# Optimization experiments

Hardware: AMD Instinct MI355X
Metric: run time of the kernel (lower is better)

The kernel has to match this reference:

```python
import jax, jax.numpy as jnp
import numpy as np

H = 256          # hidden_dim
I = 128          # input_dim
R = 32           # mod_rank
B = 16           # batch
T = 48           # timesteps
CLIP_VAL = 1.0
LN_EPS = 1e-5


def _ln(y, g, b):
    mu = jnp.mean(y, axis=-1, keepdims=True)
    var = jnp.mean((y - mu) ** 2, axis=-1, keepdims=True)
    return (y - mu) * jax.lax.rsqrt(var + LN_EPS) * g + b


def setup_inputs() -> dict:
    key = jax.random.key(0)
    ks = jax.random.split(key, 8)
    inp = {
        "x": jax.random.normal(ks[0], (T, B, I), jnp.float32),
        "h": jnp.zeros((B, H), jnp.float32),
        "v": jnp.zeros((B, H), jnp.float32),
        "dU": jnp.zeros((B, H, H), jnp.float32),
        "trace_e": jnp.zeros((B, H), jnp.float32),
        "trace_E": jnp.zeros((B, H, H), jnp.float32),
        # parameters (kaiming-ish scales; biases per reset_parameter)
        "W_x2h": jax.random.normal(ks[1], (3 * H, I), jnp.float32) * np.sqrt(2.0 / I),
        "b_x2h": jnp.zeros((3 * H,), jnp.float32),
        "W_h2h": jax.random.normal(ks[2], (3 * H, H), jnp.float32) * np.sqrt(2.0 / H),
        "b_h2h": jnp.concatenate([-jnp.ones((2 * H,)), jnp.zeros((H,))]).astype(jnp.float32),
        "ln_x_g": jnp.ones((3 * H,), jnp.float32),
        "ln_x_b": jnp.zeros((3 * H,), jnp.float32),
        "ln_h_g": jnp.ones((3 * H,), jnp.float32),
        "ln_h_b": jnp.zeros((3 * H,), jnp.float32),
        "W_h2mod": jax.random.normal(ks[3], (R, H), jnp.float32) * np.sqrt(2.0 / H),
        "b_h2mod": jnp.zeros((R,), jnp.float32),
        "W_mod2h": jax.random.normal(ks[4], (2, R), jnp.float32) * np.sqrt(2.0 / R),
        "b_mod2h": jnp.zeros((2,), jnp.float32),
        "alpha": jnp.full((1,), -4.5, jnp.float32),
        "tau_U": jnp.full((1,), -3.0, jnp.float32),
    }
    return inp


def reference(x, h, v, dU, trace_e, trace_E, W_x2h, b_x2h, W_h2h, b_h2h,
              ln_x_g, ln_x_b, ln_h_g, ln_h_b, W_h2mod, b_h2mod,
              W_mod2h, b_mod2h, alpha, tau_U):
    sp_a = jax.nn.softplus(alpha)                    # [1]
    tau = jax.nn.sigmoid(tau_U)                      # [1]
    Wv_slice = W_h2h[2 * H:3 * H, :]                 # [H,H]
    upper = jax.nn.relu(CLIP_VAL - Wv_slice) / sp_a  # [H,H], >= 0
    lower = -jax.nn.relu(CLIP_VAL + Wv_slice) / sp_a # [H,H], <= 0

    def step(carry, x_t):
        h, v, dU, te, tE = carry
        Wx = _ln(x_t @ W_x2h.T + b_x2h, ln_x_g, ln_x_b)          # [B,3H]
        Wh = h @ W_h2h.T + b_h2h                                  # [B,3H]
        plastic = sp_a * jnp.einsum('bij,bj->bi', dU, h)          # [B,H]
        Wh = Wh.at[:, 2 * H:].add(plastic)
        Wh = _ln(Wh, ln_h_g, ln_h_b)
        pre = Wx + Wh
        z = jax.nn.sigmoid(pre[:, :H])
        r = jax.nn.sigmoid(pre[:, H:2 * H])
        dv = pre[:, 2 * H:]
        v_new = (1.0 - z) * v + z * dv
        h_new = jax.nn.relu(v_new)                                # activation='relu'
        mod = jax.nn.relu(h_new @ W_h2mod.T + b_h2mod)            # [B,R]
        sm = mod @ W_mod2h.T + b_mod2h                            # [B,2]
        s = jax.nn.sigmoid(sm[:, 0:1])[:, :, None]                # [B,1,1]
        m = sm[:, 1:2][:, :, None]                                # [B,1,1]
        te_new = (1.0 - r) * te + r * h
        outer = (h_new[:, :, None] * te_new[:, None, :]
                 - te_new[:, :, None] * h_new[:, None, :])        # [B,H,H] antisym
        tE_new = (1.0 - s) * tE + s * outer
        dU_new = (1.0 - tau) * dU + tau * m * tE_new
        dU_new = jnp.minimum(dU_new, upper[None])
        dU_new = jnp.maximum(dU_new, lower[None])
        return (h_new, v_new, dU_new, te_new, tE_new), (h_new, mod)

    (h, v, dU, trace_e, trace_E), (outs, mods) = jax.lax.scan(
        step, (h, v, dU, trace_e, trace_E), x)
    return v, h, dU, trace_e, trace_E, outs, mods
```

## Files before the change

### kernel.cpp

```cpp
#include <hip/hip_runtime.h>

#define H_  256
#define I_  128
#define R_  32
#define B_  16
#define T_  48
#define H3_ 768

#define OFF_V    0
#define OFF_H    4096
#define OFF_DU   8192
#define OFF_TE   1056768
#define OFF_TT   1060864
#define OFF_OUTS 2109440
#define OFF_MODS 2306048

#define BAR_STRIDE 32

typedef unsigned long long u64;

__device__ __align__(16) float g_wx[T_*B_*H3_];
__device__ __align__(16) u64 g_whp[2*B_*H3_];
__device__ __align__(16) u64 g_plp[2*B_*H_];
__device__ int g_bar[B_*BAR_STRIDE];
__device__ int g_done[B_*BAR_STRIDE];

__device__ __forceinline__ float sigmf(float v){ return 1.0f/(1.0f+__expf(-v)); }

__device__ __forceinline__ void pstore(u64* p, int tag, float v){
  u64 u = ((u64)(unsigned)tag << 32) | (u64)__float_as_uint(v);
  __hip_atomic_store(p, u, __ATOMIC_RELAXED, __HIP_MEMORY_SCOPE_AGENT);
}
__device__ __forceinline__ u64 pload(const u64* p){
  return __hip_atomic_load((u64*)p, __ATOMIC_RELAXED, __HIP_MEMORY_SCOPE_AGENT);
}
__device__ __forceinline__ void pload4_l2(const u64* p0, const u64* p1,
                                          const u64* p2, const u64* p3,
                                          u64& u0, u64& u1, u64& u2, u64& u3){
  asm volatile(
    "global_load_dwordx2 %0, %4, off sc0\n\t"
    "global_load_dwordx2 %1, %5, off sc0\n\t"
    "global_load_dwordx2 %2, %6, off sc0\n\t"
    "global_load_dwordx2 %3, %7, off sc0\n\t"
    "s_waitcnt vmcnt(0)"
    : "=&v"(u0), "=&v"(u1), "=&v"(u2), "=&v"(u3)
    : "v"(p0), "v"(p1), "v"(p2), "v"(p3)
    : "memory");
}

__device__ __forceinline__ void groupbar_full(int* ctr, int target){
  __syncthreads();
  if (threadIdx.x == 0){
    __threadfence();
    __hip_atomic_fetch_add(ctr, 1, __ATOMIC_RELAXED, __HIP_MEMORY_SCOPE_AGENT);
    while (__hip_atomic_load(ctr, __ATOMIC_RELAXED, __HIP_MEMORY_SCOPE_AGENT) < target)
      __builtin_amdgcn_s_sleep(1);
    __threadfence();
  }
  __syncthreads();
}

__global__ __launch_bounds__(256, 1) void sgru_kernel(
    const float* __restrict__ x,     const float* __restrict__ h0,
    const float* __restrict__ v0,    const float* __restrict__ dU0,
    const float* __restrict__ te0,   const float* __restrict__ tE0,
    const float* __restrict__ Wx2h,  const float* __restrict__ bx2h,
    const float* __restrict__ Wh2h,  const float* __restrict__ bh2h,
    const float* __restrict__ lnxg,  const float* __restrict__ lnxb,
    const float* __restrict__ lnhg,  const float* __restrict__ lnhb,
    const float* __restrict__ Wh2mod,const float* __restrict__ bh2mod,
    const float* __restrict__ Wmod2h,const float* __restrict__ bmod2h,
    const float* __restrict__ alpha, const float* __restrict__ tauU,
    float* __restrict__ out)
{
  const int tid  = threadIdx.x;
  const int g    = blockIdx.x;
  const int b    = (g & 7) + 8*(g >> 7);
  const int c    = (g >> 3) & 15;
  const int lane = tid & 63;
  const int wv   = tid >> 6;

  __shared__ __align__(16) float hn_s[H_], ten_s[H_];
  __shared__ __align__(16) float xst_s[3*I_];
  __shared__ __align__(16) float lnhg_s[H3_], lnhb_s[H3_];
  __shared__ __align__(16) float wrow_s[48*256];
  __shared__ float mod_s[R_];
  __shared__ float red_s[8];

  float* ws_wx = g_wx;
  int*   ctr   = g_bar  + b*BAR_STRIDE;
  int*   dctr  = g_done + b*BAR_STRIDE;

  const float sp_a    = log1pf(__expf(alpha[0]));
  const float inv_spa = 1.0f / sp_a;
  const float tau     = sigmf(tauU[0]);

  float h_r  = h0[b*H_+tid];
  float v_r  = v0[b*H_+tid];
  float te_r = te0[b*H_+tid];
  hn_s[tid] = h_r;
  for (int idx = tid; idx < 48*64; idx += 256){
    int d = idx >> 6, j = idx & 63;
    float4 w4 = ((const float4*)(Wh2h + ((size_t)(c*48 + d))*H_))[j];
    ((float4*)wrow_s)[(d>>4)*1024 + (j>>2)*64 + (d&15)*4 + (j&3)] = w4;
  }
  for (int idx = tid; idx < H3_; idx += 256){
    lnhg_s[idx] = lnhg[idx];
    lnhb_s[idx] = lnhb[idx];
  }
  float4 upR[4], loR[4];
  float4 duR[4], tER[4];
  #pragma unroll
  for (int rr = 0; rr < 4; rr++){
    int i = c*16 + rr*4 + wv;
    float4 w = ((const float4*)(Wh2h + ((size_t)(2*H_ + i))*H_))[lane];
    upR[rr].x =  fmaxf(1.0f - w.x, 0.0f)*inv_spa;
    upR[rr].y =  fmaxf(1.0f - w.y, 0.0f)*inv_spa;
    upR[rr].z =  fmaxf(1.0f - w.z, 0.0f)*inv_spa;
    upR[rr].w =  fmaxf(1.0f - w.w, 0.0f)*inv_spa;
    loR[rr].x = -fmaxf(1.0f + w.x, 0.0f)*inv_spa;
    loR[rr].y = -fmaxf(1.0f + w.y, 0.0f)*inv_spa;
    loR[rr].z = -fmaxf(1.0f + w.z, 0.0f)*inv_spa;
    loR[rr].w = -fmaxf(1.0f + w.w, 0.0f)*inv_spa;
    size_t rowo = ((size_t)(b*H_ + i))*H_;
    duR[rr] = ((const float4*)(dU0 + rowo))[lane];
    tER[rr] = ((const float4*)(tE0 + rowo))[lane];
  }
  const int mk = tid >> 3;
  const int l8 = tid & 7;
  float4 wm[8];
  #pragma unroll
  for (int j = 0; j < 8; j++)
    wm[j] = ((const float4*)(Wh2mod + (size_t)mk*H_))[j*8 + l8];
  const float bh2m = bh2mod[mk];
  const float wmA = Wmod2h[lane & 31];
  const float wmB = Wmod2h[R_ + (lane & 31)];
  const float bm0 = bmod2h[0], bm1 = bmod2h[1];
  float bh2h_reg = 0.f;
  if (tid < 192) bh2h_reg = bh2h[c*48 + (tid>>2)];
  __syncthreads();

  {
    float* xr = xst_s;
    for (int idx = tid; idx < 3*I_; idx += 256){
      int q = idx >> 7, e = idx & 127;
      xr[q*I_ + e] = x[((size_t)((c*3+q)*B_ + b))*I_ + e];
    }
    __syncthreads();
    float acc[3][3];
    #pragma unroll
    for (int k = 0; k < 3; k++){
      acc[k][0]=0.f; acc[k][1]=0.f; acc[k][2]=0.f;
      int f = tid + 256*k;
      const float4* wr = (const float4*)(Wx2h + (size_t)f*I_);
      for (int e4 = 0; e4 < I_/4; e4++){
        float4 w4 = wr[e4];
        int e = e4*4;
        #pragma unroll
        for (int q = 0; q < 3; q++){
          float t0 = fmaf(w4.x, xr[q*I_+e],   acc[k][q]);
          t0       = fmaf(w4.y, xr[q*I_+e+1], t0);
          t0       = fmaf(w4.z, xr[q*I_+e+2], t0);
          acc[k][q]= fmaf(w4.w, xr[q*I_+e+3], t0);
        }
      }
      float bf = bx2h[f];
      acc[k][0]+=bf; acc[k][1]+=bf; acc[k][2]+=bf;
    }
    __syncthreads();
    for (int q = 0; q < 3; q++){
      float s1 = acc[0][q]+acc[1][q]+acc[2][q];
      float s2 = acc[0][q]*acc[0][q]+acc[1][q]*acc[1][q]+acc[2][q]*acc[2][q];
      #pragma unroll
      for (int off=32; off>0; off>>=1){ s1 += __shfl_xor(s1,off); s2 += __shfl_xor(s2,off); }
      if (lane==0){ red_s[wv]=s1; red_s[4+wv]=s2; }
      __syncthreads();
      s1 = red_s[0]+red_s[1]+red_s[2]+red_s[3];
      s2 = red_s[4]+red_s[5]+red_s[6]+red_s[7];
      __syncthreads();
      float mu  = s1*(1.0f/768.0f);
      float var = s2*(1.0f/768.0f) - mu*mu;
      float rs  = rsqrtf(var + 1e-5f);
      float* dst = ws_wx + ((size_t)((c*3+q)*B_ + b))*H3_;
      #pragma unroll
      for (int k = 0; k < 3; k++){
        int f = tid + 256*k;
        dst[f] = (acc[k][q]-mu)*rs*lnxg[f] + lnxb[f];
      }
    }
  }

  {
    const float4* h4 = (const float4*)hn_s;
    float4 hj = h4[lane];
    float a[4];
    #pragma unroll
    for (int rr = 0; rr < 4; rr++){
      float4 du = duR[rr];
      a[rr] = du.x*hj.x + du.y*hj.y + du.z*hj.z + du.w*hj.w;
    }
    #pragma unroll
    for (int off=32; off>0; off>>=1){
      a[0] += __shfl_xor(a[0],off); a[1] += __shfl_xor(a[1],off);
      a[2] += __shfl_xor(a[2],off); a[3] += __shfl_xor(a[3],off);
    }
    if (lane==0){
      #pragma unroll
      for (int rr = 0; rr < 4; rr++)
        pstore(&g_plp[b*H_ + c*16 + rr*4 + wv], 0, sp_a*a[rr]);
    }
    if (tid < 192){
      const int w  = tid >> 6;
      const int l4 = lane & 3;
      const float4* wb  = ((const float4*)wrow_s) + w*1024;
      const float4* hh4 = (const float4*)hn_s;
      float acc = 0.f;
      #pragma unroll
      for (int u = 0; u < 16; u++){
        float4 w4 = wb[u*64 + lane];
        float4 hv = hh4[u*4 + l4];
        acc = fmaf(w4.x,hv.x, fmaf(w4.y,hv.y, fmaf(w4.z,hv.z, fmaf(w4.w,hv.w, acc))));
      }
      acc += __shfl_xor(acc,1);
      acc += __shfl_xor(acc,2);
      if (l4==0) pstore(&g_whp[b*H3_ + c*48 + w*16 + (lane>>2)], 0, acc + bh2h_reg);
    }
  }
  groupbar_full(ctr, 16);

  for (int t = 0; t < T_; t++){
    const int p  = t & 1;
    const int pn = p ^ 1;

    const float* wxr = ws_wx + ((size_t)(t*B_ + b))*H3_;
    float wx0 = wxr[tid], wx1 = wxr[tid+256], wx2 = wxr[tid+512];

    const u64* whp = g_whp + p*(B_*H3_) + b*H3_;
    const u64* plp = g_plp + p*(B_*H_)  + b*H_;
    u64 u0, u1, u2, u3;
    int round = 0;
    for(;;){
      if ((round & 1) == 0){
        pload4_l2(whp+tid, whp+tid+256, whp+tid+512, plp+tid, u0, u1, u2, u3);
      } else {
        u0 = pload(whp + tid);
        u1 = pload(whp + tid + 256);
        u2 = pload(whp + tid + 512);
        u3 = pload(plp + tid);
      }
      bool ok = ((int)(u0>>32)==t) && ((int)(u1>>32)==t) &&
                ((int)(u2>>32)==t) && ((int)(u3>>32)==t);
      if (__all(ok)) break;
      round++;
    }
    float wh0 = __uint_as_float((unsigned)u0);
    float wh1 = __uint_as_float((unsigned)u1);
    float wh2 = __uint_as_float((unsigned)u2) + __uint_as_float((unsigned)u3);

    float hn, ten;
    {
      float s1 = wh0+wh1+wh2;
      float s2 = wh0*wh0+wh1*wh1+wh2*wh2;
      #pragma unroll
      for (int off=32; off>0; off>>=1){ s1 += __shfl_xor(s1,off); s2 += __shfl_xor(s2,off); }
      if (lane==0){ red_s[wv]=s1; red_s[4+wv]=s2; }
      __syncthreads();
      s1 = red_s[0]+red_s[1]+red_s[2]+red_s[3];
      s2 = red_s[4]+red_s[5]+red_s[6]+red_s[7];
      float mu  = s1*(1.0f/768.0f);
      float var = s2*(1.0f/768.0f) - mu*mu;
      float rs  = rsqrtf(var + 1e-5f);
      float pre0 = wx0 + (wh0-mu)*rs*lnhg_s[tid]     + lnhb_s[tid];
      float pre1 = wx1 + (wh1-mu)*rs*lnhg_s[tid+256] + lnhb_s[tid+256];
      float pre2 = wx2 + (wh2-mu)*rs*lnhg_s[tid+512] + lnhb_s[tid+512];
      float z   = sigmf(pre0);
      float r   = sigmf(pre1);
      float vn  = fmaf(z, pre2 - v_r, v_r);
      hn  = fmaxf(vn, 0.0f);
      ten = fmaf(r, h_r - te_r, te_r);
      v_r = vn; h_r = hn; te_r = ten;
      hn_s[tid] = hn; ten_s[tid] = ten;
    }
    __syncthreads();

    const float4* hn4 = (const float4*)hn_s;
    const float4* te4 = (const float4*)ten_s;
    float4 hj = hn4[lane];
    float4 tj = te4[lane];
    float hni[4], teni[4];
    #pragma unroll
    for (int rr = 0; rr < 4; rr++){
      int i = c*16 + rr*4 + wv;
      hni[rr]  = hn_s[i];
      teni[rr] = ten_s[i];
    }

    if (t < T_-1 && tid < 192){
      const int w  = tid >> 6;
      const int l4 = lane & 3;
      const float4* wb  = ((const float4*)wrow_s) + w*1024;
      float acc = 0.f;
      #pragma unroll
      for (int u = 0; u < 16; u++){
        float4 w4 = wb[u*64 + lane];
        float4 hv = hn4[u*4 + l4];
        acc = fmaf(w4.x,hv.x, fmaf(w4.y,hv.y, fmaf(w4.z,hv.z, fmaf(w4.w,hv.w, acc))));
      }
      acc += __shfl_xor(acc,1);
      acc += __shfl_xor(acc,2);
      if (l4==0) pstore(&g_whp[pn*(B_*H3_) + b*H3_ + c*48 + w*16 + (lane>>2)],
                        t+1, acc + bh2h_reg);
    }

    {
      float acc = 0.f;
      #pragma unroll
      for (int j = 0; j < 8; j++){
        float4 hv = hn4[j*8 + l8];
        float4 w4 = wm[j];
        acc = fmaf(w4.x,hv.x, fmaf(w4.y,hv.y, fmaf(w4.z,hv.z, fmaf(w4.w,hv.w, acc))));
      }
      acc += __shfl_xor(acc,1); acc += __shfl_xor(acc,2); acc += __shfl_xor(acc,4);
      if (l8==0) mod_s[mk] = fmaxf(acc + bh2m, 0.0f);
    }
    __syncthreads();

    float s_b, m_b;
    {
      float mv = mod_s[lane & 31];
      float p0 = mv*wmA, p1 = mv*wmB;
      #pragma unroll
      for (int off=16; off>0; off>>=1){ p0 += __shfl_xor(p0,off); p1 += __shfl_xor(p1,off); }
      s_b = sigmf(p0 + bm0);
      m_b = p1 + bm1;
    }

    float pacc[4];
    #pragma unroll
    for (int rr = 0; rr < 4; rr++){
      float4 du = duR[rr];
      float4 tE = tER[rr];
      float4 up = upR[rr];
      float4 lo = loR[rr];
      float h_i = hni[rr], t_i = teni[rr];
      float4 nd, nt;
      float acc;
      { float o_ = h_i*tj.x - t_i*hj.x;
        float tn = fmaf(s_b, o_ - tE.x, tE.x);
        float dn = fmaf(tau, fmaf(m_b, tn, -du.x), du.x);
        dn = fminf(dn, up.x); dn = fmaxf(dn, lo.x);
        nt.x = tn; nd.x = dn; acc = dn*hj.x; }
      { float o_ = h_i*tj.y - t_i*hj.y;
        float tn = fmaf(s_b, o_ - tE.y, tE.y);
        float dn = fmaf(tau, fmaf(m_b, tn, -du.y), du.y);
        dn = fminf(dn, up.y); dn = fmaxf(dn, lo.y);
        nt.y = tn; nd.y = dn; acc = fmaf(dn, hj.y, acc); }
      { float o_ = h_i*tj.z - t_i*hj.z;
        float tn = fmaf(s_b, o_ - tE.z, tE.z);
        float dn = fmaf(tau, fmaf(m_b, tn, -du.z), du.z);
        dn = fminf(dn, up.z); dn = fmaxf(dn, lo.z);
        nt.z = tn; nd.z = dn; acc = fmaf(dn, hj.z, acc); }
      { float o_ = h_i*tj.w - t_i*hj.w;
        float tn = fmaf(s_b, o_ - tE.w, tE.w);
        float dn = fmaf(tau, fmaf(m_b, tn, -du.w), du.w);
        dn = fminf(dn, up.w); dn = fmaxf(dn, lo.w);
        nt.w = tn; nd.w = dn; acc = fmaf(dn, hj.w, acc); }
      duR[rr] = nd;
      tER[rr] = nt;
      pacc[rr] = acc;
    }
    #pragma unroll
    for (int off=32; off>0; off>>=1){
      pacc[0] += __shfl_xor(pacc[0],off); pacc[1] += __shfl_xor(pacc[1],off);
      pacc[2] += __shfl_xor(pacc[2],off); pacc[3] += __shfl_xor(pacc[3],off);
    }
    if (t < T_-1 && lane==0){
      u64* pd = g_plp + pn*(B_*H_) + b*H_ + c*16 + wv;
      pstore(pd + 0,  t+1, sp_a*pacc[0]);
      pstore(pd + 4,  t+1, sp_a*pacc[1]);
      pstore(pd + 8,  t+1, sp_a*pacc[2]);
      pstore(pd + 12, t+1, sp_a*pacc[3]);
    }

    if (tid < 16) out[OFF_OUTS + ((size_t)(t*B_+b))*H_ + c*16 + tid] = hn_s[c*16 + tid];
    if (tid < 2)  out[OFF_MODS + ((size_t)(t*B_+b))*R_ + c*2 + tid]  = mod_s[c*2 + tid];
    if (t == T_-1){
      #pragma unroll
      for (int rr = 0; rr < 4; rr++){
        int i = c*16 + rr*4 + wv;
        size_t rowo = ((size_t)(b*H_ + i))*H_;
        ((float4*)(out + OFF_DU + rowo))[lane] = duR[rr];
        ((float4*)(out + OFF_TT + rowo))[lane] = tER[rr];
      }
      if (c == 0){
        out[OFF_V  + b*H_ + tid] = v_r;
        out[OFF_H  + b*H_ + tid] = h_r;
        out[OFF_TE + b*H_ + tid] = te_r;
      }
    }
  }

  __syncthreads();
  if (threadIdx.x == 0){
    int d = __hip_atomic_fetch_add(dctr, 1, __ATOMIC_RELAXED, __HIP_MEMORY_SCOPE_AGENT);
    if (d == 15){
      __hip_atomic_store(ctr,  0, __ATOMIC_RELAXED, __HIP_MEMORY_SCOPE_AGENT);
      __hip_atomic_store(dctr, 0, __ATOMIC_RELAXED, __HIP_MEMORY_SCOPE_AGENT);
    }
  }
}

extern "C" void kernel_launch(void* const* d_in, const int* in_sizes, int n_in,
                              void* d_out, int out_size, void* d_ws, size_t ws_size,
                              hipStream_t stream)
{
  const float* x      = (const float*)d_in[0];
  const float* h0     = (const float*)d_in[1];
  const float* v0     = (const float*)d_in[2];
  const float* dU0    = (const float*)d_in[3];
  const float* te0    = (const float*)d_in[4];
  const float* tE0    = (const float*)d_in[5];
  const float* Wx2h   = (const float*)d_in[6];
  const float* bx2h   = (const float*)d_in[7];
  const float* Wh2h   = (const float*)d_in[8];
  const float* bh2h   = (const float*)d_in[9];
  const float* lnxg   = (const float*)d_in[10];
  const float* lnxb   = (const float*)d_in[11];
  const float* lnhg   = (const float*)d_in[12];
  const float* lnhb   = (const float*)d_in[13];
  const float* Wh2mod = (const float*)d_in[14];
  const float* bh2mod = (const float*)d_in[15];
  const float* Wmod2h = (const float*)d_in[16];
  const float* bmod2h = (const float*)d_in[17];
  const float* alpha  = (const float*)d_in[18];
  const float* tauU   = (const float*)d_in[19];
  float* out = (float*)d_out;

  sgru_kernel<<<dim3(256), dim3(256), 0, stream>>>(
      x, h0, v0, dU0, te0, tE0, Wx2h, bx2h, Wh2h, bh2h,
      lnxg, lnxb, lnhg, lnhb, Wh2mod, bh2mod, Wmod2h, bmod2h,
      alpha, tauU, out);
}
```

Measured before the change: 280.0 us.

## Replace shuffle reductions with DPP row reductions and reorder mod computation

Swaps the __shfl_xor butterfly reductions for DPP row_shr and row_bcast sequences whose result lands in lane 63, so the writer lanes become 63 or the last lane of each group. The modulation matvec and the antisymmetric outer product are moved ahead of the W_h2h partial matvec, so the block barrier and the s/m broadcast happen earlier. The poll loop now favours the sc0 L2 loads on three of every four rounds. The 0.5 factor in the s/m step offsets the wavefront-wide sum over the 32-entry mod vector, which is duplicated across both halves of the wave. This relies on exact DPP control encodings and row masks, which is a correctness risk.

```diff
diff --git a/kernel.cpp b/kernel.cpp
--- a/kernel.cpp
+++ b/kernel.cpp
@@ -26,6 +26,32 @@
 __device__ int g_done[B_*BAR_STRIDE];
 
 __device__ __forceinline__ float sigmf(float v){ return 1.0f/(1.0f+__expf(-v)); }
+
+#define DPPADD(x, ctrl, rmask) \
+  x += __int_as_float(__builtin_amdgcn_update_dpp(0, __float_as_int(x), ctrl, rmask, 0xf, false))
+__device__ __forceinline__ float wred(float x){
+  DPPADD(x, 0x111, 0xf);
+  DPPADD(x, 0x112, 0xf);
+  DPPADD(x, 0x114, 0xf);
+  DPPADD(x, 0x118, 0xf);
+  DPPADD(x, 0x142, 0xa);
+  DPPADD(x, 0x143, 0xc);
+  return x;
+}
+__device__ __forceinline__ float red8(float x){
+  DPPADD(x, 0x111, 0xf);
+  DPPADD(x, 0x112, 0xf);
+  DPPADD(x, 0x114, 0xf);
+  return x;
+}
+__device__ __forceinline__ float red4(float x){
+  DPPADD(x, 0x111, 0xf);
+  DPPADD(x, 0x112, 0xf);
+  return x;
+}
+__device__ __forceinline__ float bcast63(float x){
+  return __int_as_float(__builtin_amdgcn_readlane(__float_as_int(x), 63));
+}
 
 __device__ __forceinline__ void pstore(u64* p, int tag, float v){
   u64 u = ((u64)(unsigned)tag << 32) | (u64)__float_as_uint(v);
@@ -171,9 +197,8 @@
     for (int q = 0; q < 3; q++){
       float s1 = acc[0][q]+acc[1][q]+acc[2][q];
       float s2 = acc[0][q]*acc[0][q]+acc[1][q]*acc[1][q]+acc[2][q]*acc[2][q];
-      #pragma unroll
-      for (int off=32; off>0; off>>=1){ s1 += __shfl_xor(s1,off); s2 += __shfl_xor(s2,off); }
-      if (lane==0){ red_s[wv]=s1; red_s[4+wv]=s2; }
+      s1 = wred(s1); s2 = wred(s2);
+      if (lane==63){ red_s[wv]=s1; red_s[4+wv]=s2; }
       __syncthreads();
       s1 = red_s[0]+red_s[1]+red_s[2]+red_s[3];
       s2 = red_s[4]+red_s[5]+red_s[6]+red_s[7];
@@ -198,13 +223,9 @@
     for (int rr = 0; rr < 4; rr++){
       float4 du = duR[rr];
       a[rr] = du.x*hj.x + du.y*hj.y + du.z*hj.z + du.w*hj.w;
-    }
-    #pragma unroll
-    for (int off=32; off>0; off>>=1){
-      a[0] += __shfl_xor(a[0],off); a[1] += __shfl_xor(a[1],off);
-      a[2] += __shfl_xor(a[2],off); a[3] += __shfl_xor(a[3],off);
-    }
-    if (lane==0){
+      a[rr] = wred(a[rr]);
+    }
+    if (lane==63){
       #pragma unroll
       for (int rr = 0; rr < 4; rr++)
         pstore(&g_plp[b*H_ + c*16 + rr*4 + wv], 0, sp_a*a[rr]);
@@ -221,9 +242,8 @@
         float4 hv = hh4[u*4 + l4];
         acc = fmaf(w4.x,hv.x, fmaf(w4.y,hv.y, fmaf(w4.z,hv.z, fmaf(w4.w,hv.w, acc))));
       }
-      acc += __shfl_xor(acc,1);
-      acc += __shfl_xor(acc,2);
-      if (l4==0) pstore(&g_whp[b*H3_ + c*48 + w*16 + (lane>>2)], 0, acc + bh2h_reg);
+      acc = red4(acc);
+      if ((lane&3)==3) pstore(&g_whp[b*H3_ + c*48 + w*16 + (lane>>2)], 0, acc + bh2h_reg);
     }
   }
   groupbar_full(ctr, 16);
@@ -240,7 +260,7 @@
     u64 u0, u1, u2, u3;
     int round = 0;
     for(;;){
-      if ((round & 1) == 0){
+      if ((round & 3) != 3){
         pload4_l2(whp+tid, whp+tid+256, whp+tid+512, plp+tid, u0, u1, u2, u3);
       } else {
         u0 = pload(whp + tid);
@@ -261,9 +281,8 @@
     {
       float s1 = wh0+wh1+wh2;
       float s2 = wh0*wh0+wh1*wh1+wh2*wh2;
-      #pragma unroll
-      for (int off=32; off>0; off>>=1){ s1 += __shfl_xor(s1,off); s2 += __shfl_xor(s2,off); }
-      if (lane==0){ red_s[wv]=s1; red_s[4+wv]=s2; }
+      s1 = wred(s1); s2 = wred(s2);
+      if (lane==63){ red_s[wv]=s1; red_s[4+wv]=s2; }
       __syncthreads();
       s1 = red_s[0]+red_s[1]+red_s[2]+red_s[3];
       s2 = red_s[4]+red_s[5]+red_s[6]+red_s[7];
@@ -295,6 +314,36 @@
       teni[rr] = ten_s[i];
     }
 
+    {
+      float macc = 0.f;
+      #pragma unroll
+      for (int j = 0; j < 8; j++){
+        float4 hv = hn4[j*8 + l8];
+        float4 w4 = wm[j];
+        macc = fmaf(w4.x,hv.x, fmaf(w4.y,hv.y, fmaf(w4.z,hv.z, fmaf(w4.w,hv.w, macc))));
+      }
+      macc = red8(macc);
+      if (l8==7) mod_s[mk] = fmaxf(macc + bh2m, 0.0f);
+    }
+    float4 oR[4];
+    #pragma unroll
+    for (int rr = 0; rr < 4; rr++){
+      oR[rr].x = hni[rr]*tj.x - teni[rr]*hj.x;
+      oR[rr].y = hni[rr]*tj.y - teni[rr]*hj.y;
+      oR[rr].z = hni[rr]*tj.z - teni[rr]*hj.z;
+      oR[rr].w = hni[rr]*tj.w - teni[rr]*hj.w;
+    }
+    __syncthreads();
+
+    float s_b, m_b;
+    {
+      float mv = mod_s[lane & 31];
+      float p0 = mv*wmA, p1 = mv*wmB;
+      p0 = wred(p0); p1 = wred(p1);
+      s_b = sigmf(0.5f*bcast63(p0) + bm0);
+      m_b = 0.5f*bcast63(p1) + bm1;
+    }
+
     if (t < T_-1 && tid < 192){
       const int w  = tid >> 6;
       const int l4 = lane & 3;
@@ -306,33 +355,9 @@
         float4 hv = hn4[u*4 + l4];
         acc = fmaf(w4.x,hv.x, fmaf(w4.y,hv.y, fmaf(w4.z,hv.z, fmaf(w4.w,hv.w, acc))));
       }
-      acc += __shfl_xor(acc,1);
-      acc += __shfl_xor(acc,2);
-      if (l4==0) pstore(&g_whp[pn*(B_*H3_) + b*H3_ + c*48 + w*16 + (lane>>2)],
-                        t+1, acc + bh2h_reg);
-    }
-
-    {
-      float acc = 0.f;
-      #pragma unroll
-      for (int j = 0; j < 8; j++){
-        float4 hv = hn4[j*8 + l8];
-        float4 w4 = wm[j];
-        acc = fmaf(w4.x,hv.x, fmaf(w4.y,hv.y, fmaf(w4.z,hv.z, fmaf(w4.w,hv.w, acc))));
-      }
-      acc += __shfl_xor(acc,1); acc += __shfl_xor(acc,2); acc += __shfl_xor(acc,4);
-      if (l8==0) mod_s[mk] = fmaxf(acc + bh2m, 0.0f);
-    }
-    __syncthreads();
-
-    float s_b, m_b;
-    {
-      float mv = mod_s[lane & 31];
-      float p0 = mv*wmA, p1 = mv*wmB;
-      #pragma unroll
-      for (int off=16; off>0; off>>=1){ p0 += __shfl_xor(p0,off); p1 += __shfl_xor(p1,off); }
-      s_b = sigmf(p0 + bm0);
-      m_b = p1 + bm1;
+      acc = red4(acc);
+      if ((lane&3)==3) pstore(&g_whp[pn*(B_*H3_) + b*H3_ + c*48 + w*16 + (lane>>2)],
+                              t+1, acc + bh2h_reg);
     }
 
     float pacc[4];
@@ -342,26 +367,22 @@
       float4 tE = tER[rr];
       float4 up = upR[rr];
       float4 lo = loR[rr];
-      float h_i = hni[rr], t_i = teni[rr];
+      float4 o  = oR[rr];
       float4 nd, nt;
       float acc;
-      { float o_ = h_i*tj.x - t_i*hj.x;
-        float tn = fmaf(s_b, o_ - tE.x, tE.x);
+      { float tn = fmaf(s_b, o.x - tE.x, tE.x);
         float dn = fmaf(tau, fmaf(m_b, tn, -du.x), du.x);
         dn = fminf(dn, up.x); dn = fmaxf(dn, lo.x);
         nt.x = tn; nd.x = dn; acc = dn*hj.x; }
-      { float o_ = h_i*tj.y - t_i*hj.y;
-        float tn = fmaf(s_b, o_ - tE.y, tE.y);
+      { float tn = fmaf(s_b, o.y - tE.y, tE.y);
         float dn = fmaf(tau, fmaf(m_b, tn, -du.y), du.y);
         dn = fminf(dn, up.y); dn = fmaxf(dn, lo.y);
         nt.y = tn; nd.y = dn; acc = fmaf(dn, hj.y, acc); }
-      { float o_ = h_i*tj.z - t_i*hj.z;
-        float tn = fmaf(s_b, o_ - tE.z, tE.z);
+      { float tn = fmaf(s_b, o.z - tE.z, tE.z);
         float dn = fmaf(tau, fmaf(m_b, tn, -du.z), du.z);
         dn = fminf(dn, up.z); dn = fmaxf(dn, lo.z);
         nt.z = tn; nd.z = dn; acc = fmaf(dn, hj.z, acc); }
-      { float o_ = h_i*tj.w - t_i*hj.w;
-        float tn = fmaf(s_b, o_ - tE.w, tE.w);
+      { float tn = fmaf(s_b, o.w - tE.w, tE.w);
         float dn = fmaf(tau, fmaf(m_b, tn, -du.w), du.w);
         dn = fminf(dn, up.w); dn = fmaxf(dn, lo.w);
         nt.w = tn; nd.w = dn; acc = fmaf(dn, hj.w, acc); }
@@ -369,12 +390,9 @@
       tER[rr] = nt;
       pacc[rr] = acc;
     }
-    #pragma unroll
-    for (int off=32; off>0; off>>=1){
-      pacc[0] += __shfl_xor(pacc[0],off); pacc[1] += __shfl_xor(pacc[1],off);
-      pacc[2] += __shfl_xor(pacc[2],off); pacc[3] += __shfl_xor(pacc[3],off);
-    }
-    if (t < T_-1 && lane==0){
+    pacc[0] = wred(pacc[0]); pacc[1] = wred(pacc[1]);
+    pacc[2] = wred(pacc[2]); pacc[3] = wred(pacc[3]);
+    if (t < T_-1 && lane==63){
       u64* pd = g_plp + pn*(B_*H_) + b*H_ + c*16 + wv;
       pstore(pd + 0,  t+1, sp_a*pacc[0]);
       pstore(pd + 4,  t+1, sp_a*pacc[1]);
```

Measured after the change: 303.0 us. 8.2% more time.
